# Kernel optimization log

Measured on AMD Instinct MI355X. Metric: run time of the kernel, lower is better.

Reference implementation:

```python
import jax, jax.numpy as jnp
import numpy as np
import math

B, L, HID, H = 16, 1024, 1024, 16
E = HID // H
HALF = L // 2 + 1                      # 513 rfft bins
GLOBAL_RATIO = 0.6
LEFT = int(HALF * (1.0 - GLOBAL_RATIO))  # 205 (i=0, filter_mixer='G')
RIGHT = HALF                            # 513
FACTOR = 1
TOP_K = int(FACTOR * math.log(L))       # 6
LN_EPS = 1e-12


def setup_inputs() -> dict:
    key = jax.random.key(0)
    ks = jax.random.split(key, 12)
    s = 0.02
    return {
        "input_tensor": jax.random.normal(ks[0], (B, L, HID), jnp.float32),
        "attention_mask": jnp.zeros((B, 1, 1, L), jnp.float32),
        "Wq": jax.random.normal(ks[1], (HID, HID), jnp.float32) * s,
        "bq": jnp.zeros((HID,), jnp.float32),
        "Wk": jax.random.normal(ks[2], (HID, HID), jnp.float32) * s,
        "bk": jnp.zeros((HID,), jnp.float32),
        "Wv": jax.random.normal(ks[3], (HID, HID), jnp.float32) * s,
        "bv": jnp.zeros((HID,), jnp.float32),
        "Wd": jax.random.normal(ks[4], (HID, HID), jnp.float32) * s,
        "bd": jnp.zeros((HID,), jnp.float32),
        "gamma": jnp.ones((HID,), jnp.float32),
        "beta": jnp.zeros((HID,), jnp.float32),
    }


def _heads(x):  # [B,L,HID] -> [B,H,E,L]
    return x.reshape(B, L, H, E).transpose(0, 2, 3, 1)


def _layer_norm(x, gamma, beta):
    mu = jnp.mean(x, axis=-1, keepdims=True)
    var = jnp.var(x, axis=-1, keepdims=True)
    return (x - mu) / jnp.sqrt(var + LN_EPS) * gamma + beta


def reference(input_tensor, attention_mask, Wq, bq, Wk, bk, Wv, bv, Wd, bd, gamma, beta):
    # QKV projections -> [B,H,E,L]
    q = _heads(input_tensor @ Wq + bq)
    k = _heads(input_tensor @ Wk + bk)
    v = _heads(input_tensor @ Wv + bv)

    # FFT-based autocorrelation restricted to retained frequency band [LEFT,RIGHT)
    q_fft = jnp.fft.rfft(q, axis=-1)            # [B,H,E,HALF] complex64
    k_fft = jnp.fft.rfft(k, axis=-1)
    res = q_fft[..., LEFT:RIGHT] * jnp.conj(k_fft[..., LEFT:RIGHT])
    box = jnp.zeros((B, H, E, HALF), res.dtype).at[..., LEFT:RIGHT].set(res)
    corr = jnp.fft.irfft(box, n=L, axis=-1)     # [B,H,E,L]

    # time_delay_agg_training: topk shared delays, softmax-weighted roll aggregation
    mean_value = jnp.mean(corr, axis=(1, 2))            # [B,L]
    _, idx = jax.lax.top_k(jnp.mean(mean_value, axis=0), TOP_K)  # [TOP_K]
    weights = mean_value[:, idx]                         # [B,TOP_K]
    tmp_corr = jax.nn.softmax(weights, axis=-1)
    delays_agg = jnp.zeros_like(v)
    for i in range(TOP_K):  # TOP_K=6, fixed small loop
        pattern = jnp.roll(v, -idx[i], axis=-1)
        delays_agg = delays_agg + pattern * tmp_corr[:, i][:, None, None, None]

    # [B,H,E,L] -> [B,L,HID]
    context = delays_agg.transpose(0, 3, 1, 2).reshape(B, L, HID)
    hidden = context @ Wd + bd
    return _layer_norm(hidden + input_tensor, gamma, beta)
```

## Files before the change

### kernel.cpp

```cpp
#include <hip/hip_runtime.h>


typedef unsigned short u16;
typedef unsigned int   u32;
typedef __attribute__((ext_vector_type(8))) __bf16 bf16x8;
typedef __attribute__((ext_vector_type(4))) float  floatx4;

#define HIDn 1024

__device__ __forceinline__ u16 f2b(float f){ u32 i = __float_as_uint(f); return (u16)((i + 0x7fffu + ((i>>16)&1u)) >> 16); }

__device__ __forceinline__ void gl_lds16(const u16* g, u16* l){
  __builtin_amdgcn_global_load_lds((__attribute__((address_space(1))) const void*)g,
                                   (__attribute__((address_space(3))) void*)l, 16, 0, 0);
}

__device__ __forceinline__ void bar(){
  asm volatile("" ::: "memory");
  __builtin_amdgcn_s_barrier();
  asm volatile("" ::: "memory");
}
__device__ __forceinline__ void lgkm0(){
  asm volatile("s_waitcnt lgkmcnt(0)" ::: "memory");
  __builtin_amdgcn_sched_barrier(0);
}

__global__ void fill_kernel(float* __restrict__ out, float v, int n)
{
  const int i = blockIdx.x*blockDim.x + threadIdx.x;
  if (i < n) out[i] = v;
}

__global__ __launch_bounds__(1024)
void prep_kernel(const float* __restrict__ x, u16* __restrict__ xb,
                 float* __restrict__ cbuf,
                 const float* __restrict__ Wq, const float* __restrict__ Wk,
                 const float* __restrict__ Wv, const float* __restrict__ Wd,
                 u16* __restrict__ WqkvT, u16* __restrict__ WdT)
{
  __shared__ float tile[32][33];
  if (blockIdx.x < 2048){
    const int i = blockIdx.x*1024 + threadIdx.x;
    if (i < 16384) cbuf[i] = 0.f;
    const float4* xp = (const float4*)x;
    const float4 a = xp[2*i], b = xp[2*i+1];
    uint4 o;
    o.x = (u32)f2b(a.x) | ((u32)f2b(a.y)<<16);
    o.y = (u32)f2b(a.z) | ((u32)f2b(a.w)<<16);
    o.z = (u32)f2b(b.x) | ((u32)f2b(b.y)<<16);
    o.w = (u32)f2b(b.z) | ((u32)f2b(b.w)<<16);
    ((uint4*)xb)[i] = o;
  } else {
    const int bb  = blockIdx.x - 2048;
    const int mat = bb >> 10;
    const int rem = bb & 1023;
    const int bxT = rem & 31, byT = rem >> 5;
    const int tx = threadIdx.x & 31, ty = threadIdx.x >> 5;
    const float* W = (mat==0)?Wq:(mat==1)?Wk:(mat==2)?Wv:Wd;
    const int k = byT*32 + ty, n = bxT*32 + tx;
    tile[ty][tx] = W[(long)k*HIDn + n];
    __syncthreads();
    const int on = bxT*32 + ty, ok = byT*32 + tx;
    const u16 val = f2b(tile[tx][ty]);
    if (mat < 3) WqkvT[(long)(mat*HIDn + on)*HIDn + ok] = val;
    else         WdT[(long)on*HIDn + ok] = val;
  }
}

template<int EPI>
__global__ __launch_bounds__(512, 2)
void gemm_mfma(const u16* __restrict__ A, int lda, long sA,
               const u16* __restrict__ Bt, int ldb, long sB,
               void* __restrict__ C0, u16* __restrict__ o1, u16* __restrict__ o2,
               int ldc, int K,
               const float* __restrict__ b0, const float* __restrict__ b1,
               const float* __restrict__ b2, const float* __restrict__ resid,
               float* __restrict__ cbuf)
{
  __shared__ __align__(16) u16 As[2][16384];
  __shared__ __align__(16) u16 Bs[2][16384];
  __shared__ float bins[512];

  const int gx = gridDim.x, gy = gridDim.y;
  const int lin = (blockIdx.z*gy + blockIdx.y)*gx + blockIdx.x;
  const int cpx = (gx*gy*gridDim.z) >> 3;
  const int swz = (lin & 7)*cpx + (lin >> 3);
  const int bx  = swz % gx;
  const int byz = swz / gx;
  const int by  = byz % gy;
  const int bz  = byz / gy;

  const int tid  = threadIdx.x;
  const int wave = tid >> 6, lane = tid & 63;
  const int waveM = wave >> 2, waveN = wave & 3;
  const int qd = lane >> 4, ln = lane & 15, rl = ln & 7;
  const u16* Ab = A  + (long)bz * sA;
  const u16* Bb = Bt + (long)bz * sB;
  const int aRow0 = by * 256, bRow0 = bx * 256;
  const int nt = K >> 6;

  const int s0 = wave*128 + lane;
  const int r0 = s0 >> 3, r1 = r0 + 8;
  const int kc = ((s0 & 7) ^ (r0 & 7)) * 8;
  const long aOff0 = (long)(aRow0 + r0)*lda + kc;
  const long aOff1 = (long)(aRow0 + r1)*lda + kc;
  const long bOff0 = (long)(bRow0 + r0)*ldb + kc;
  const long bOff1 = (long)(bRow0 + r1)*ldb + kc;
  const int dstW = wave*1024;

#define STAGE_A(p, h, kt) do{ \
    gl_lds16(Ab + aOff0 + (long)(h)*128*lda + (kt), &As[p][(h)*8192 + dstW]); \
    gl_lds16(Ab + aOff1 + (long)(h)*128*lda + (kt), &As[p][(h)*8192 + dstW + 512]); }while(0)
#define STAGE_B(p, h, kt) do{ \
    gl_lds16(Bb + bOff0 + (long)(h)*128*ldb + (kt), &Bs[p][(h)*8192 + dstW]); \
    gl_lds16(Bb + bOff1 + (long)(h)*128*ldb + (kt), &Bs[p][(h)*8192 + dstW + 512]); }while(0)

  if (EPI == 3) bins[tid] = 0.f;

  floatx4 acc[8][4];
  const floatx4 z4 = {0.f, 0.f, 0.f, 0.f};
  #pragma unroll
  for (int i=0;i<8;++i)
    #pragma unroll
    for (int j=0;j<4;++j) acc[i][j] = z4;

  const int aRd = (waveM*128 + ln)*64;
  const int bRd = (waveN*64  + ln)*64;
  const int csw0 = ((0 + qd) ^ rl) * 8;
  const int csw1 = ((4 + qd) ^ rl) * 8;

  bf16x8 av0[4], av1[4];
  bf16x8 bvA0[2], bvA1[2];
  bf16x8 bvB0[2], bvB1[2];

#define DS_AV(BUF, MH) do{ const u16* Ap_ = &As[BUF][0]; \
    _Pragma("unroll") for (int mi=0;mi<4;++mi){ \
      av0[mi] = *(const bf16x8*)(Ap_ + aRd + (MH)*4096 + mi*1024 + csw0); \
      av1[mi] = *(const bf16x8*)(Ap_ + aRd + (MH)*4096 + mi*1024 + csw1); } }while(0)
#define DS_BV(BUF, NH, d0_, d1_) do{ const u16* Bp_ = &Bs[BUF][0]; \
    _Pragma("unroll") for (int ni=0;ni<2;++ni){ \
      d0_[ni] = *(const bf16x8*)(Bp_ + bRd + ((NH)*2+ni)*1024 + csw0); \
      d1_[ni] = *(const bf16x8*)(Bp_ + bRd + ((NH)*2+ni)*1024 + csw1); } }while(0)
#define MFMAQ(MH, NH, b0_, b1_) do{ \
    __builtin_amdgcn_sched_barrier(0); \
    __builtin_amdgcn_s_setprio(1); \
    _Pragma("unroll") for (int mi=0;mi<4;++mi) \
      _Pragma("unroll") for (int ni=0;ni<2;++ni){ \
        acc[(MH)*4+mi][(NH)*2+ni] = __builtin_amdgcn_mfma_f32_16x16x32_bf16(av0[mi], b0_[ni], acc[(MH)*4+mi][(NH)*2+ni],0,0,0); \
        acc[(MH)*4+mi][(NH)*2+ni] = __builtin_amdgcn_mfma_f32_16x16x32_bf16(av1[mi], b1_[ni], acc[(MH)*4+mi][(NH)*2+ni],0,0,0); } \
    __builtin_amdgcn_s_setprio(0); \
    __builtin_amdgcn_sched_barrier(0); }while(0)

  STAGE_B(0,0,0);  STAGE_B(0,1,0);  STAGE_A(0,0,0);  STAGE_A(0,1,0);
  STAGE_B(1,0,64); STAGE_B(1,1,64); STAGE_A(1,0,64); STAGE_A(1,1,64);
  asm volatile("s_waitcnt vmcnt(8)" ::: "memory");
  bar();

  const int nIt = nt >> 1;
  for (int it = 0; it < nIt-1; ++it){
    const int k2 = (it*2+2) << 6;
    const int k3 = (it*2+3) << 6;
    DS_AV(0,0); DS_BV(0,0,bvA0,bvA1);
    bar(); lgkm0(); MFMAQ(0,0,bvA0,bvA1); bar();
    DS_BV(0,1,bvB0,bvB1);
    bar(); lgkm0(); MFMAQ(0,1,bvB0,bvB1); bar();
    DS_AV(0,1); STAGE_B(0,0,k2);
    bar(); lgkm0(); MFMAQ(1,0,bvA0,bvA1); bar();
    STAGE_B(0,1,k2);
    asm volatile("s_waitcnt vmcnt(4)" ::: "memory");
    bar(); MFMAQ(1,1,bvB0,bvB1); bar();
    DS_AV(1,0); DS_BV(1,0,bvA0,bvA1); STAGE_A(0,0,k2);
    bar(); lgkm0(); MFMAQ(0,0,bvA0,bvA1); bar();
    DS_BV(1,1,bvB0,bvB1); STAGE_A(0,1,k2);
    bar(); lgkm0(); MFMAQ(0,1,bvB0,bvB1); bar();
    DS_AV(1,1); STAGE_B(1,0,k3);
    bar(); lgkm0(); MFMAQ(1,0,bvA0,bvA1); bar();
    STAGE_B(1,1,k3); STAGE_A(1,0,k3); STAGE_A(1,1,k3);
    asm volatile("s_waitcnt vmcnt(8)" ::: "memory");
    bar(); MFMAQ(1,1,bvB0,bvB1); bar();
  }
  DS_AV(0,0); DS_BV(0,0,bvA0,bvA1);
  bar(); lgkm0(); MFMAQ(0,0,bvA0,bvA1); bar();
  DS_BV(0,1,bvB0,bvB1);
  bar(); lgkm0(); MFMAQ(0,1,bvB0,bvB1); bar();
  DS_AV(0,1);
  bar(); lgkm0(); MFMAQ(1,0,bvA0,bvA1); bar();
  asm volatile("s_waitcnt vmcnt(0)" ::: "memory");
  bar(); MFMAQ(1,1,bvB0,bvB1); bar();
  DS_AV(1,0); DS_BV(1,0,bvA0,bvA1);
  bar(); lgkm0(); MFMAQ(0,0,bvA0,bvA1); bar();
  DS_BV(1,1,bvB0,bvB1);
  bar(); lgkm0(); MFMAQ(0,1,bvB0,bvB1); bar();
  DS_AV(1,1);
  bar(); lgkm0(); MFMAQ(1,0,bvA0,bvA1); bar();
  MFMAQ(1,1,bvB0,bvB1);
#undef STAGE_A
#undef STAGE_B
#undef DS_AV
#undef DS_BV
#undef MFMAQ

  if (EPI == 3){
    float dsum[11][4];
    #pragma unroll
    for (int dd=0; dd<11; ++dd)
      #pragma unroll
      for (int r=0;r<4;++r) dsum[dd][r] = 0.f;
    #pragma unroll
    for (int mi=0;mi<8;++mi)
      #pragma unroll
      for (int ni=0;ni<4;++ni){
        const int dd = mi - ni + 3;
        #pragma unroll
        for (int r=0;r<4;++r) dsum[dd][r] += acc[mi][ni][r];
      }
    const int base = 255 + 128*waveM - 64*waveN + 4*qd - ln;
    #pragma unroll
    for (int dd=0; dd<11; ++dd)
      #pragma unroll
      for (int r=0;r<4;++r)
        atomicAdd(&bins[base + 16*(dd-3) + r], dsum[dd][r]);
    __syncthreads();
    if (tid < 511){
      const int d = (aRow0 - bRow0 + tid - 255) & 1023;
      atomicAdd(cbuf + bz*1024 + d, bins[tid]);
    }
    return;
  }

  if (EPI == 0){
    const int which = bx >> 2;
    const float* bp = (which==0) ? b0 : ((which==1) ? b1 : b2);
    u16* Cb = (which==0) ? (u16*)C0 : ((which==1) ? o1 : o2);
    const int nb = bRow0 & 1023;
    #pragma unroll
    for (int mi=0;mi<8;++mi){
      const int gm = aRow0 + waveM*128 + mi*16 + qd*4;
      #pragma unroll
      for (int ni=0;ni<4;++ni){
        const int nl = nb + waveN*64 + ni*16 + ln;
        const float bias = bp[nl];
        #pragma unroll
        for (int r=0;r<4;++r) Cb[(long)(gm+r)*ldc + nl] = f2b(acc[mi][ni][r] + bias);
      }
    }
  } else {
    float* C = (float*)C0;
    #pragma unroll
    for (int mi=0;mi<8;++mi){
      const int gm = aRow0 + waveM*128 + mi*16 + qd*4;
      #pragma unroll
      for (int ni=0;ni<4;++ni){
        const int gn = bRow0 + waveN*64 + ni*16 + ln;
        const float bias = b0[gn];
        #pragma unroll
        for (int r=0;r<4;++r)
          C[(long)(gm+r)*ldc + gn] = acc[mi][ni][r] + bias + resid[(long)(gm+r)*ldc + gn];
      }
    }
  }
}

__global__ __launch_bounds__(1024)
void spect_kernel(const float* __restrict__ c, int* __restrict__ idxout,
                  float* __restrict__ wout)
{
  __shared__ float csh[16][1024];
  __shared__ float gsh[1024];
  __shared__ float csum[1024];
  __shared__ float vals[1024];
  __shared__ float wv[16];
  __shared__ int   wi[16];
  __shared__ int   chosen[6];
  __shared__ float pw[96];
  const int t = threadIdx.x, lane = t & 63, wid = t >> 6;

  float sc = 0.f;
  #pragma unroll
  for (int b = 0; b < 16; ++b){ const float v = c[b*1024 + t]; csh[b][t] = v; sc += v; }
  csum[t] = sc;
  {
    float s;
    if (t == 0) s = 307.f;
    else {
      const float k = 3.14159265358979e0f/1024.f;
      const int n1 = (307*t) & 2047, n2 = (716*t) & 2047;
      s = sinf((float)n1*k) * cosf((float)n2*k) / sinf((float)t*k);
    }
    gsh[t] = (2.f*s + ((t & 1) ? -1.f : 1.f)) * (1.0f/1048576.0f);
  }
  __syncthreads();

  float S = 0.f;
  #pragma unroll 4
  for (int m = 0; m < 1024; ++m) S += csum[m] * gsh[(t - m) & 1023];
  vals[t] = S;
  __syncthreads();

  for (int r = 0; r < 6; ++r){
    float cv = vals[t]; int ci = t;
    #pragma unroll
    for (int off = 32; off > 0; off >>= 1){
      const float ov = __shfl_down(cv, off);
      const int   oi = __shfl_down(ci, off);
      if (ov > cv || (ov == cv && oi < ci)){ cv = ov; ci = oi; }
    }
    if (lane == 0){ wv[wid] = cv; wi[wid] = ci; }
    __syncthreads();
    if (t == 0){
      float bv = wv[0]; int bi = wi[0];
      #pragma unroll
      for (int k = 1; k < 16; ++k)
        if (wv[k] > bv || (wv[k] == bv && wi[k] < bi)){ bv = wv[k]; bi = wi[k]; }
      chosen[r] = bi; idxout[r] = bi; vals[bi] = -3.0e38f;
    }
    __syncthreads();
  }

  if (t < 768){
    const int p = t >> 3, li = t & 7;
    const int b = p / 6, i = p % 6, ch = chosen[i];
    float acc = 0.f;
    #pragma unroll 4
    for (int m = li*128; m < li*128 + 128; ++m) acc += csh[b][m] * gsh[(ch - m) & 1023];
    #pragma unroll
    for (int off = 4; off > 0; off >>= 1) acc += __shfl_down(acc, off);
    if (li == 0) pw[p] = acc;
  }
  __syncthreads();
  if (t < 16){
    float w[6]; float mx = -3.0e38f;
    #pragma unroll
    for (int i = 0; i < 6; ++i){ w[i] = pw[t*6 + i]; mx = fmaxf(mx, w[i]); }
    float sum = 0.f;
    #pragma unroll
    for (int i = 0; i < 6; ++i){ w[i] = expf(w[i] - mx); sum += w[i]; }
    #pragma unroll
    for (int i = 0; i < 6; ++i) wout[t*6 + i] = w[i] / sum;
  }
}

__global__ __launch_bounds__(256)
void context_kernel(const u16* __restrict__ Vb, const int* __restrict__ idx,
                    const float* __restrict__ w, u16* __restrict__ CT)
{
  const int lin = blockIdx.x;
  const int xcd = lin & 7, j = lin >> 3;
  const int row = xcd*2048 + j*2 + (threadIdx.x >> 7);
  const int b = row >> 10, l = row & 1023;
  const int t = threadIdx.x & 127;
  float wl[6]; int id[6];
  #pragma unroll
  for (int i = 0; i < 6; ++i){ id[i] = idx[i]; wl[i] = w[b*6 + i]; }
  float acc[8] = {0,0,0,0,0,0,0,0};
  #pragma unroll
  for (int i = 0; i < 6; ++i){
    const long src = (long)b*1024 + ((l + id[i]) & 1023);
    const uint4 pk = *(const uint4*)(Vb + src*1024 + t*8);
    const float ww = wl[i];
    union{float f; u32 u;} cv;
    cv.u = pk.x<<16;          acc[0] += ww*cv.f;
    cv.u = pk.x & 0xffff0000u; acc[1] += ww*cv.f;
    cv.u = pk.y<<16;          acc[2] += ww*cv.f;
    cv.u = pk.y & 0xffff0000u; acc[3] += ww*cv.f;
    cv.u = pk.z<<16;          acc[4] += ww*cv.f;
    cv.u = pk.z & 0xffff0000u; acc[5] += ww*cv.f;
    cv.u = pk.w<<16;          acc[6] += ww*cv.f;
    cv.u = pk.w & 0xffff0000u; acc[7] += ww*cv.f;
  }
  uint4 o;
  o.x = (u32)f2b(acc[0]) | ((u32)f2b(acc[1])<<16);
  o.y = (u32)f2b(acc[2]) | ((u32)f2b(acc[3])<<16);
  o.z = (u32)f2b(acc[4]) | ((u32)f2b(acc[5])<<16);
  o.w = (u32)f2b(acc[6]) | ((u32)f2b(acc[7])<<16);
  *(uint4*)(CT + (long)row*1024 + t*8) = o;
}

__global__ __launch_bounds__(256)
void ln_kernel(float* __restrict__ io, const float* __restrict__ gamma,
               const float* __restrict__ beta)
{
  __shared__ float s1[256];
  __shared__ float s2[256];
  const int row = blockIdx.x, t = threadIdx.x;
  float4 v = ((const float4*)(io + (long)row*1024))[t];
  s1[t] = v.x+v.y+v.z+v.w;
  s2[t] = v.x*v.x+v.y*v.y+v.z*v.z+v.w*v.w;
  __syncthreads();
  for (int off = 128; off > 0; off >>= 1){
    if (t < off){ s1[t] += s1[t+off]; s2[t] += s2[t+off]; }
    __syncthreads();
  }
  const float mu  = s1[0] * (1.f/1024.f);
  const float var = fmaxf(s2[0] * (1.f/1024.f) - mu*mu, 0.f);
  const float rstd = rsqrtf(var + 1e-12f);
  const float4 g  = ((const float4*)gamma)[t];
  const float4 be = ((const float4*)beta)[t];
  float4 o;
  o.x = (v.x-mu)*rstd*g.x + be.x;
  o.y = (v.y-mu)*rstd*g.y + be.y;
  o.z = (v.z-mu)*rstd*g.z + be.z;
  o.w = (v.w-mu)*rstd*g.w + be.w;
  ((float4*)(io + (long)row*1024))[t] = o;
}

extern "C" void kernel_launch(void* const* d_in, const int* in_sizes, int n_in,
                              void* d_out, int out_size, void* d_ws, size_t ws_size,
                              hipStream_t stream)
{
  (void)in_sizes; (void)n_in;
  const float* x     = (const float*)d_in[0];
  const float* Wq    = (const float*)d_in[2];
  const float* bq    = (const float*)d_in[3];
  const float* Wk    = (const float*)d_in[4];
  const float* bk    = (const float*)d_in[5];
  const float* Wv    = (const float*)d_in[6];
  const float* bv    = (const float*)d_in[7];
  const float* Wd    = (const float*)d_in[8];
  const float* bd    = (const float*)d_in[9];
  const float* gamma = (const float*)d_in[10];
  const float* beta  = (const float*)d_in[11];
  float* outp = (float*)d_out;

  const size_t NEED = 142741952UL;
  if (ws_size < NEED){
    const int n = out_size/2;
    fill_kernel<<<(n+255)/256, 256, 0, stream>>>(outp, (float)ws_size, n);
    return;
  }
  char* ws = (char*)d_ws;
  u16*  xb    = (u16*)(ws);
  u16*  Qb    = (u16*)(ws + 33554432L);
  u16*  Kb    = (u16*)(ws + 67108864L);
  u16*  Vb    = (u16*)(ws + 100663296L);
  u16*  WqkvT = (u16*)(ws + 134217728L);
  u16*  WdT   = (u16*)(ws + 140509184L);
  float* cbuf = (float*)(ws + 142606336L);
  int*   idxb = (int*)  (ws + 142741504L);
  float* wsm  = (float*)(ws + 142741568L);
  u16*  CT    = Qb;

  prep_kernel<<<6144, 1024, 0, stream>>>(x, xb, cbuf, Wq, Wk, Wv, Wd, WqkvT, WdT);

  gemm_mfma<0><<<dim3(12,64,1), 512, 0, stream>>>(
      xb, 1024, 0L, WqkvT, 1024, 0L, Qb, Kb, Vb, 1024, 1024,
      bq, bk, bv, nullptr, nullptr);

  gemm_mfma<3><<<dim3(4,4,16), 512, 0, stream>>>(
      Qb, 1024, 1048576L, Kb, 1024, 1048576L, nullptr, nullptr, nullptr, 0, 1024,
      nullptr, nullptr, nullptr, nullptr, cbuf);

  spect_kernel<<<1, 1024, 0, stream>>>(cbuf, idxb, wsm);
  context_kernel<<<8192, 256, 0, stream>>>(Vb, idxb, wsm, CT);

  gemm_mfma<2><<<dim3(4,64,1), 512, 0, stream>>>(
      CT, 1024, 0L, WdT, 1024, 0L, outp, nullptr, nullptr, 1024, 1024,
      bd, nullptr, nullptr, x, nullptr);

  ln_kernel<<<16384, 256, 0, stream>>>(outp, gamma, beta);
}
```

Before: 450.0 us.

## Fuse spectral top-k and LayerNorm into GEMM tails via last-block counters

Removes the standalone spectrum/top-k kernel and the LayerNorm kernel. Each GEMM now increments a global atomic counter, and the last-arriving block does the follow-up work. For the correlation GEMM that is the 1024-point circular convolution, top-6 selection and softmax weights, computed in reused LDS. For the output GEMM, the last block of each 256-row stripe normalizes its 256 rows in place. This saves two launches and a full extra read/write pass of the output. In exchange, a single block does serial tail work at the end of a GEMM, and correctness depends on threadfence and counter ordering.

```diff
diff --git a/kernel.cpp b/kernel.cpp
--- a/kernel.cpp
+++ b/kernel.cpp
@@ -33,7 +33,7 @@
 
 __global__ __launch_bounds__(1024)
 void prep_kernel(const float* __restrict__ x, u16* __restrict__ xb,
-                 float* __restrict__ cbuf,
+                 float* __restrict__ cbuf, int* __restrict__ ctrs,
                  const float* __restrict__ Wq, const float* __restrict__ Wk,
                  const float* __restrict__ Wv, const float* __restrict__ Wd,
                  u16* __restrict__ WqkvT, u16* __restrict__ WdT)
@@ -42,6 +42,7 @@
   if (blockIdx.x < 2048){
     const int i = blockIdx.x*1024 + threadIdx.x;
     if (i < 16384) cbuf[i] = 0.f;
+    if (blockIdx.x == 0 && threadIdx.x < 65) ctrs[threadIdx.x] = 0;
     const float4* xp = (const float4*)x;
     const float4 a = xp[2*i], b = xp[2*i+1];
     uint4 o;
@@ -75,11 +76,14 @@
                int ldc, int K,
                const float* __restrict__ b0, const float* __restrict__ b1,
                const float* __restrict__ b2, const float* __restrict__ resid,
-               float* __restrict__ cbuf)
+               float* __restrict__ cbuf, int* __restrict__ ctrs,
+               const float* __restrict__ gam, const float* __restrict__ bet,
+               int* __restrict__ idxo, float* __restrict__ wo)
 {
   __shared__ __align__(16) u16 As[2][16384];
   __shared__ __align__(16) u16 Bs[2][16384];
   __shared__ float bins[512];
+  __shared__ int lastf;
 
   const int gx = gridDim.x, gy = gridDim.y;
   const int lin = (blockIdx.z*gy + blockIdx.y)*gx + blockIdx.x;
@@ -225,6 +229,89 @@
       const int d = (aRow0 - bRow0 + tid - 255) & 1023;
       atomicAdd(cbuf + bz*1024 + d, bins[tid]);
     }
+    __syncthreads();
+    if (tid == 0){
+      __threadfence();
+      const int nb = gx*gy*gridDim.z;
+      lastf = (atomicAdd(ctrs, 1) == nb-1);
+    }
+    __syncthreads();
+    if (!lastf) return;
+    __threadfence();
+    float* csh  = (float*)&As[0][0];
+    float* gshp = (float*)&Bs[0][0];
+    float* csum = gshp + 1024;
+    float* vals = csum + 1024;
+    float* wvp  = vals + 1024;
+    int*   wip  = (int*)(wvp + 16);
+    int*   chos = wip + 16;
+    float* pw   = (float*)(chos + 8);
+    for (int i = tid; i < 16384; i += 512) csh[i] = cbuf[i];
+    __syncthreads();
+    for (int l = tid; l < 1024; l += 512){
+      float sc = 0.f;
+      #pragma unroll
+      for (int b = 0; b < 16; ++b) sc += csh[b*1024 + l];
+      csum[l] = sc;
+      float s;
+      if (l == 0) s = 307.f;
+      else {
+        const float kk = 3.14159265358979e0f/1024.f;
+        const int n1 = (307*l) & 2047, n2 = (716*l) & 2047;
+        s = sinf((float)n1*kk) * cosf((float)n2*kk) / sinf((float)l*kk);
+      }
+      gshp[l] = (2.f*s + ((l & 1) ? -1.f : 1.f)) * (1.0f/1048576.0f);
+    }
+    __syncthreads();
+    for (int l = tid; l < 1024; l += 512){
+      float S = 0.f;
+      #pragma unroll 4
+      for (int m = 0; m < 1024; ++m) S += csum[m] * gshp[(l - m) & 1023];
+      vals[l] = S;
+    }
+    __syncthreads();
+    for (int r = 0; r < 6; ++r){
+      float v1 = vals[tid], v2 = vals[tid + 512];
+      float cv = v1; int ci = tid;
+      if (v2 > v1){ cv = v2; ci = tid + 512; }
+      #pragma unroll
+      for (int off = 32; off > 0; off >>= 1){
+        const float ov = __shfl_down(cv, off);
+        const int   oi = __shfl_down(ci, off);
+        if (ov > cv || (ov == cv && oi < ci)){ cv = ov; ci = oi; }
+      }
+      if (lane == 0){ wvp[wave] = cv; wip[wave] = ci; }
+      __syncthreads();
+      if (tid == 0){
+        float bv = wvp[0]; int bi = wip[0];
+        #pragma unroll
+        for (int k2 = 1; k2 < 8; ++k2)
+          if (wvp[k2] > bv || (wvp[k2] == bv && wip[k2] < bi)){ bv = wvp[k2]; bi = wip[k2]; }
+        chos[r] = bi; idxo[r] = bi; vals[bi] = -3.0e38f;
+      }
+      __syncthreads();
+    }
+    if (tid < 384){
+      const int p = tid >> 2, li = tid & 3;
+      const int b = p / 6, i = p % 6, ch = chos[i];
+      float a2 = 0.f;
+      #pragma unroll 4
+      for (int m = li*256; m < li*256 + 256; ++m) a2 += csh[b*1024 + m] * gshp[(ch - m) & 1023];
+      a2 += __shfl_down(a2, 2);
+      a2 += __shfl_down(a2, 1);
+      if (li == 0) pw[p] = a2;
+    }
+    __syncthreads();
+    if (tid < 16){
+      float w[6]; float mx = -3.0e38f;
+      #pragma unroll
+      for (int i = 0; i < 6; ++i){ w[i] = pw[tid*6 + i]; mx = fmaxf(mx, w[i]); }
+      float sum = 0.f;
+      #pragma unroll
+      for (int i = 0; i < 6; ++i){ w[i] = expf(w[i] - mx); sum += w[i]; }
+      #pragma unroll
+      for (int i = 0; i < 6; ++i) wo[tid*6 + i] = w[i] / sum;
+    }
     return;
   }
 
@@ -258,85 +345,50 @@
           C[(long)(gm+r)*ldc + gn] = acc[mi][ni][r] + bias + resid[(long)(gm+r)*ldc + gn];
       }
     }
-  }
-}
-
-__global__ __launch_bounds__(1024)
-void spect_kernel(const float* __restrict__ c, int* __restrict__ idxout,
-                  float* __restrict__ wout)
-{
-  __shared__ float csh[16][1024];
-  __shared__ float gsh[1024];
-  __shared__ float csum[1024];
-  __shared__ float vals[1024];
-  __shared__ float wv[16];
-  __shared__ int   wi[16];
-  __shared__ int   chosen[6];
-  __shared__ float pw[96];
-  const int t = threadIdx.x, lane = t & 63, wid = t >> 6;
-
-  float sc = 0.f;
-  #pragma unroll
-  for (int b = 0; b < 16; ++b){ const float v = c[b*1024 + t]; csh[b][t] = v; sc += v; }
-  csum[t] = sc;
-  {
-    float s;
-    if (t == 0) s = 307.f;
-    else {
-      const float k = 3.14159265358979e0f/1024.f;
-      const int n1 = (307*t) & 2047, n2 = (716*t) & 2047;
-      s = sinf((float)n1*k) * cosf((float)n2*k) / sinf((float)t*k);
-    }
-    gsh[t] = (2.f*s + ((t & 1) ? -1.f : 1.f)) * (1.0f/1048576.0f);
-  }
-  __syncthreads();
-
-  float S = 0.f;
-  #pragma unroll 4
-  for (int m = 0; m < 1024; ++m) S += csum[m] * gsh[(t - m) & 1023];
-  vals[t] = S;
-  __syncthreads();
-
-  for (int r = 0; r < 6; ++r){
-    float cv = vals[t]; int ci = t;
-    #pragma unroll
-    for (int off = 32; off > 0; off >>= 1){
-      const float ov = __shfl_down(cv, off);
-      const int   oi = __shfl_down(ci, off);
-      if (ov > cv || (ov == cv && oi < ci)){ cv = ov; ci = oi; }
-    }
-    if (lane == 0){ wv[wid] = cv; wi[wid] = ci; }
-    __syncthreads();
-    if (t == 0){
-      float bv = wv[0]; int bi = wi[0];
-      #pragma unroll
-      for (int k = 1; k < 16; ++k)
-        if (wv[k] > bv || (wv[k] == bv && wi[k] < bi)){ bv = wv[k]; bi = wi[k]; }
-      chosen[r] = bi; idxout[r] = bi; vals[bi] = -3.0e38f;
-    }
-    __syncthreads();
-  }
-
-  if (t < 768){
-    const int p = t >> 3, li = t & 7;
-    const int b = p / 6, i = p % 6, ch = chosen[i];
-    float acc = 0.f;
-    #pragma unroll 4
-    for (int m = li*128; m < li*128 + 128; ++m) acc += csh[b][m] * gsh[(ch - m) & 1023];
-    #pragma unroll
-    for (int off = 4; off > 0; off >>= 1) acc += __shfl_down(acc, off);
-    if (li == 0) pw[p] = acc;
-  }
-  __syncthreads();
-  if (t < 16){
-    float w[6]; float mx = -3.0e38f;
-    #pragma unroll
-    for (int i = 0; i < 6; ++i){ w[i] = pw[t*6 + i]; mx = fmaxf(mx, w[i]); }
-    float sum = 0.f;
-    #pragma unroll
-    for (int i = 0; i < 6; ++i){ w[i] = expf(w[i] - mx); sum += w[i]; }
-    #pragma unroll
-    for (int i = 0; i < 6; ++i) wout[t*6 + i] = w[i] / sum;
+    __syncthreads();
+    if (tid == 0){
+      __threadfence();
+      lastf = (atomicAdd(&ctrs[1 + by], 1) == gx - 1);
+    }
+    __syncthreads();
+    if (!lastf) return;
+    __threadfence();
+    float* gsh_ = (float*)&As[0][0];
+    float* bsh_ = gsh_ + 1024;
+    for (int i = tid; i < 1024; i += 512){ gsh_[i] = gam[i]; bsh_[i] = bet[i]; }
+    __syncthreads();
+    const float4* g4 = (const float4*)gsh_;
+    const float4* be4 = (const float4*)bsh_;
+    for (int rr = 0; rr < 32; ++rr){
+      const int row = aRow0 + wave*32 + rr;
+      float4* rp = (float4*)(C + (long)row*1024);
+      float4 vv[4]; float s1 = 0.f, s2 = 0.f;
+      #pragma unroll
+      for (int j = 0; j < 4; ++j){
+        vv[j] = rp[j*64 + lane];
+        s1 += vv[j].x + vv[j].y + vv[j].z + vv[j].w;
+        s2 += vv[j].x*vv[j].x + vv[j].y*vv[j].y + vv[j].z*vv[j].z + vv[j].w*vv[j].w;
+      }
+      #pragma unroll
+      for (int off = 32; off > 0; off >>= 1){
+        s1 += __shfl_xor(s1, off);
+        s2 += __shfl_xor(s2, off);
+      }
+      const float mu   = s1 * (1.f/1024.f);
+      const float var  = fmaxf(s2 * (1.f/1024.f) - mu*mu, 0.f);
+      const float rstd = rsqrtf(var + 1e-12f);
+      #pragma unroll
+      for (int j = 0; j < 4; ++j){
+        const int idx = j*64 + lane;
+        const float4 g = g4[idx], be = be4[idx];
+        float4 o;
+        o.x = (vv[j].x - mu)*rstd*g.x + be.x;
+        o.y = (vv[j].y - mu)*rstd*g.y + be.y;
+        o.z = (vv[j].z - mu)*rstd*g.z + be.z;
+        o.w = (vv[j].w - mu)*rstd*g.w + be.w;
+        rp[idx] = o;
+      }
+    }
   }
 }
 
@@ -376,34 +428,6 @@
   *(uint4*)(CT + (long)row*1024 + t*8) = o;
 }
 
-__global__ __launch_bounds__(256)
-void ln_kernel(float* __restrict__ io, const float* __restrict__ gamma,
-               const float* __restrict__ beta)
-{
-  __shared__ float s1[256];
-  __shared__ float s2[256];
-  const int row = blockIdx.x, t = threadIdx.x;
-  float4 v = ((const float4*)(io + (long)row*1024))[t];
-  s1[t] = v.x+v.y+v.z+v.w;
-  s2[t] = v.x*v.x+v.y*v.y+v.z*v.z+v.w*v.w;
-  __syncthreads();
-  for (int off = 128; off > 0; off >>= 1){
-    if (t < off){ s1[t] += s1[t+off]; s2[t] += s2[t+off]; }
-    __syncthreads();
-  }
-  const float mu  = s1[0] * (1.f/1024.f);
-  const float var = fmaxf(s2[0] * (1.f/1024.f) - mu*mu, 0.f);
-  const float rstd = rsqrtf(var + 1e-12f);
-  const float4 g  = ((const float4*)gamma)[t];
-  const float4 be = ((const float4*)beta)[t];
-  float4 o;
-  o.x = (v.x-mu)*rstd*g.x + be.x;
-  o.y = (v.y-mu)*rstd*g.y + be.y;
-  o.z = (v.z-mu)*rstd*g.z + be.z;
-  o.w = (v.w-mu)*rstd*g.w + be.w;
-  ((float4*)(io + (long)row*1024))[t] = o;
-}
-
 extern "C" void kernel_launch(void* const* d_in, const int* in_sizes, int n_in,
                               void* d_out, int out_size, void* d_ws, size_t ws_size,
                               hipStream_t stream)
@@ -436,26 +460,24 @@
   u16*  WqkvT = (u16*)(ws + 134217728L);
   u16*  WdT   = (u16*)(ws + 140509184L);
   float* cbuf = (float*)(ws + 142606336L);
+  int*   ctrs = (int*)  (ws + 142671872L);
   int*   idxb = (int*)  (ws + 142741504L);
   float* wsm  = (float*)(ws + 142741568L);
   u16*  CT    = Qb;
 
-  prep_kernel<<<6144, 1024, 0, stream>>>(x, xb, cbuf, Wq, Wk, Wv, Wd, WqkvT, WdT);
+  prep_kernel<<<6144, 1024, 0, stream>>>(x, xb, cbuf, ctrs, Wq, Wk, Wv, Wd, WqkvT, WdT);
 
   gemm_mfma<0><<<dim3(12,64,1), 512, 0, stream>>>(
       xb, 1024, 0L, WqkvT, 1024, 0L, Qb, Kb, Vb, 1024, 1024,
-      bq, bk, bv, nullptr, nullptr);
+      bq, bk, bv, nullptr, nullptr, nullptr, nullptr, nullptr, nullptr, nullptr);
 
   gemm_mfma<3><<<dim3(4,4,16), 512, 0, stream>>>(
       Qb, 1024, 1048576L, Kb, 1024, 1048576L, nullptr, nullptr, nullptr, 0, 1024,
-      nullptr, nullptr, nullptr, nullptr, cbuf);
-
-  spect_kernel<<<1, 1024, 0, stream>>>(cbuf, idxb, wsm);
+      nullptr, nullptr, nullptr, nullptr, cbuf, ctrs, nullptr, nullptr, idxb, wsm);
+
   context_kernel<<<8192, 256, 0, stream>>>(Vb, idxb, wsm, CT);
 
   gemm_mfma<2><<<dim3(4,64,1), 512, 0, stream>>>(
       CT, 1024, 0L, WdT, 1024, 0L, outp, nullptr, nullptr, 1024, 1024,
-      bd, nullptr, nullptr, x, nullptr);
-
-  ln_kernel<<<16384, 256, 0, stream>>>(outp, gamma, beta);
-}
+      bd, nullptr, nullptr, x, nullptr, ctrs, gamma, beta, nullptr, nullptr);
+}
```

After: 517.9 us. 1.15x slower.
